# Optimization experiments

Measured on AMD Instinct MI355X. Metric: run time of the kernel, lower is better.

## Reference

```python
import jax, jax.numpy as jnp
import numpy as np

# Sinabs LIF semantics (norm_input=True default):
#   v[t] = alpha * v[t-1] + (1 - alpha) * x[t],  alpha = exp(-1/tau_mem)
#   spikes = MultiSpike: max(floor(v / threshold), 0)   (default sa.ActivationFunction)
#   reset  = MembraneSubtract: v -= spikes * threshold
# threshold_low=None -> no lower clamp.

TAU_MEM = 20.0
THRESHOLD = 1.0
GRAD_WIDTH = 0.5   # sinabs SingleExponential surrogate defaults
GRAD_SCALE = 1.0

@jax.custom_vjp
def spike_fn(v):
    # MultiSpike: number of threshold crossings this step
    return jnp.maximum(jnp.floor(v / THRESHOLD), 0.0)

def _spike_fwd(v):
    return spike_fn(v), v

def _spike_bwd(v, g):
    # single-exponential surrogate gradient around threshold
    sg = (GRAD_SCALE / GRAD_WIDTH) * jnp.exp(-jnp.abs(v - THRESHOLD) / GRAD_WIDTH)
    return (g * sg,)

spike_fn.defvjp(_spike_fwd, _spike_bwd)

def lif_layer(x):
    # x: [B, T, N] synaptic input; returns spikes [B, T, N]
    alpha = jnp.exp(jnp.asarray(-1.0 / TAU_MEM, dtype=x.dtype))
    one_m = 1.0 - alpha

    def step(v, xt):
        v = alpha * v + one_m * xt
        s = spike_fn(v)
        v = v - s * THRESHOLD  # membrane subtract reset
        return v, s

    v0 = jnp.zeros(x.shape[:1] + x.shape[2:], dtype=x.dtype)  # [B, N]
    _, spikes = jax.lax.scan(step, v0, jnp.swapaxes(x, 0, 1))  # scan over T
    return jnp.swapaxes(spikes, 0, 1)

def setup_inputs() -> dict:
    key = jax.random.key(0)
    k0, k1, k2, k3 = jax.random.split(key, 4)
    B, T, C_IN = 256, 4096, 16
    data = jax.random.normal(k0, (B, T, C_IN), dtype=jnp.float32)
    # nn.Linear(in, out, bias=False) weights are [out, in], kaiming-uniform-ish scale
    w1 = jax.random.normal(k1, (16, 16), dtype=jnp.float32) / np.sqrt(16)
    w2 = jax.random.normal(k2, (32, 16), dtype=jnp.float32) / np.sqrt(16)
    w3 = jax.random.normal(k3, (10, 32), dtype=jnp.float32) / np.sqrt(32)
    return {"data": data, "w1": w1, "w2": w2, "w3": w3}

def reference(data, w1, w2, w3):
    out = jnp.einsum('btc,oc->bto', data, w1)
    out = lif_layer(out)
    out = jnp.einsum('btc,oc->bto', out, w2)
    out = lif_layer(out)
    out = jnp.einsum('btc,oc->bto', out, w3)
    out = lif_layer(out)
    return out
```

## Files before the change

kernel.cpp:

```cpp
#include <hip/hip_runtime.h>
#include <stdint.h>
#include <math.h>

#define T_STEPS 4096
#define BATCH   256
#define NB_BLK  256

#define WAIT_VM0   0x0F70
#define WAIT_LGKM0 0xC07F

__device__ __forceinline__ float lif_step(float& v, float xs, float alpha) {
    float vp = fmaf(alpha, v, xs);
    float fr = vp - floorf(vp);
    float vn = fminf(vp, fr);
    float s  = vp - vn;
    v = vn;
    return s;
}

__device__ __forceinline__ float ubf(uint32_t w, int k) {
    return (float)((w >> (k * 8)) & 0xffu);
}

__device__ __forceinline__ float dot16(const float wr[16],
    float4 c0, float4 c1, float4 c2, float4 c3)
{
    float p0 = fmaf(wr[1], c0.y, wr[0] * c0.x);
    p0 = fmaf(wr[2], c0.z, p0);  p0 = fmaf(wr[3], c0.w, p0);
    float p1 = fmaf(wr[5], c1.y, wr[4] * c1.x);
    p1 = fmaf(wr[6], c1.z, p1);  p1 = fmaf(wr[7], c1.w, p1);
    float p2 = fmaf(wr[9], c2.y, wr[8] * c2.x);
    p2 = fmaf(wr[10], c2.z, p2); p2 = fmaf(wr[11], c2.w, p2);
    float p3 = fmaf(wr[13], c3.y, wr[12] * c3.x);
    p3 = fmaf(wr[14], c3.z, p3); p3 = fmaf(wr[15], c3.w, p3);
    return (p0 + p1) + (p2 + p3);
}

__device__ __forceinline__ void load_lds16(const float* g, float* l) {
    __builtin_amdgcn_global_load_lds(
        (const __attribute__((address_space(1))) void*)g,
        (__attribute__((address_space(3))) void*)l, 16, 0, 0);
}


__global__ __launch_bounds__(1024) void seg1(
    const float* __restrict__ x, const float* __restrict__ w1,
    float* __restrict__ out, uint8_t* __restrict__ s1t,
    uint8_t* __restrict__ bm1, uint8_t* __restrict__ bm2,
    uint8_t* __restrict__ flag1, uint8_t* __restrict__ flag2,
    float alpha, float one_m, float alpha16)
{
    const int tid = threadIdx.x;
    const int b   = blockIdx.x;

    __shared__ __align__(16) float xbuf[16640];
    __shared__ float   sh_end[NB_BLK][16];
    __shared__ float   sh_m0[NB_BLK][16];
    __shared__ float   sh_m1[NB_BLK][16];
    __shared__ uint8_t sh_badseg[16][NB_BLK];
    __shared__ int     sh_badch;
    __shared__ int     sh_spike;

    const int co = tid & 15;
    const int sg = tid >> 4;
    const int wv = tid >> 6;
    const int ln = tid & 63;

    const float* xb = x + (size_t)b * T_STEPS * 16;

#pragma unroll
    for (int q = 0; q < 4; ++q) {
        int s = wv * 4 + q;
        load_lds16(xb + (size_t)s * 256 + ln * 4, &xbuf[s * 260 + ln * 4]);
    }

    float4* o4 = (float4*)(out + (size_t)b * T_STEPS * 10);
    float4 z4 = make_float4(0.f, 0.f, 0.f, 0.f);
#pragma unroll
    for (int i = 0; i < 10; ++i) o4[i * 1024 + tid] = z4;
    if (tid < 16)
        ((uint4*)(bm1 + (size_t)b * NB_BLK))[tid] = make_uint4(0u,0u,0u,0u);
    else if (tid < 32)
        ((uint4*)(bm2 + (size_t)b * NB_BLK))[tid - 16] = make_uint4(0u,0u,0u,0u);
    else if (tid == 32) { flag2[b] = 0; sh_badch = 0; sh_spike = 0; }

    float wr[16];
#pragma unroll
    for (int i = 0; i < 16; ++i) wr[i] = one_m * w1[co * 16 + i];

    const int sbase = sg * 260;
    for (int k = 0; k < 4; ++k) {
        __builtin_amdgcn_s_waitcnt(WAIT_VM0);

        float acc = 0.0f, m0 = -1e30f, m1 = -1e30f, pw = alpha;
#pragma unroll
        for (int j = 0; j < 16; ++j) {
            const float* rp = &xbuf[sbase + j * 16];
            float4 c0 = *(const float4*)(rp + 0);
            float4 c1 = *(const float4*)(rp + 4);
            float4 c2 = *(const float4*)(rp + 8);
            float4 c3 = *(const float4*)(rp + 12);
            float y = dot16(wr, c0, c1, c2, c3);
            acc = fmaf(alpha, acc, y);
            m0  = fmaxf(m0, acc);
            m1  = fmaxf(m1, acc + pw);
            pw *= alpha;
        }
        const int gs = k * 64 + sg;
        sh_end[gs][co] = acc;
        sh_m0[gs][co]  = m0;
        sh_m1[gs][co]  = m1;

        if (k < 3) {
            __builtin_amdgcn_s_waitcnt(WAIT_LGKM0);
#pragma unroll
            for (int q = 0; q < 4; ++q) {
                int s = wv * 4 + q;
                load_lds16(xb + (size_t)((k + 1) * 64 + s) * 256 + ln * 4,
                           &xbuf[s * 260 + ln * 4]);
            }
        }
    }
    __syncthreads();

    if (tid < 16) {
        const int c = tid;
        float vs = 0.0f;
        int bad = 0;
#pragma unroll 8
        for (int s = 0; s < NB_BLK; ++s) {
            float vsu = fminf(fmaxf(vs + 1e-3f, 0.0f), 1.0f);
            float bound = fmaf(1.0f - vsu, sh_m0[s][c], vsu * sh_m1[s][c]);
            int sb = (bound >= 0.999f) ? 1 : 0;
            sh_badseg[c][s] = (uint8_t)sb;
            bad |= sb;
            vs = fmaf(alpha16, vs, sh_end[s][c]);
        }
        if (bad) atomicOr(&sh_badch, 1 << c);
    }
    __syncthreads();

    const int badmask = sh_badch;
    if (badmask) {
        uint4* sz = (uint4*)(s1t + (size_t)b * 16 * T_STEPS);
#pragma unroll
        for (int i = 0; i < 4; ++i) sz[i * 1024 + tid] = make_uint4(0u,0u,0u,0u);
        __syncthreads();

        int m = badmask;
        for (int i = 0; i < wv; ++i) m &= m - 1;
        if (ln == 0 && m) {
            const int c = __ffs(m) - 1;
            float wc[16];
#pragma unroll
            for (int i = 0; i < 16; ++i) wc[i] = one_m * w1[c * 16 + i];
            uint8_t* op  = s1t + ((size_t)b * 16 + c) * T_STEPS;
            uint8_t* bmp = bm1 + (size_t)b * NB_BLK;
            const uint8_t* bs = &sh_badseg[c][0];
            float v = 0.0f;
            int any = 0;
            for (int s = 0; s < NB_BLK; ++s) {
                if (!bs[s]) {
                    v = fmaf(alpha16, v, sh_end[s][c]);
                } else {
                    const float4* xq = (const float4*)xb + (size_t)s * 64;
                    uint32_t w[4] = {0u,0u,0u,0u};
#pragma unroll 4
                    for (int j = 0; j < 16; ++j) {
                        float4 c0 = xq[j*4+0], c1 = xq[j*4+1];
                        float4 c2 = xq[j*4+2], c3 = xq[j*4+3];
                        float y  = dot16(wc, c0, c1, c2, c3);
                        float sp = lif_step(v, y, alpha);
                        w[j >> 2] |= ((uint32_t)(int)sp) << ((j & 3) * 8);
                    }
                    if (w[0] | w[1] | w[2] | w[3]) {
                        *(uint4*)(op + s * 16) = make_uint4(w[0], w[1], w[2], w[3]);
                        bmp[s] = 1;
                        any = 1;
                    }
                }
            }
            if (any) sh_spike = 1;
        }
        __syncthreads();
    }
    if (tid == 0) flag1[b] = (uint8_t)sh_spike;
}

__global__ __launch_bounds__(64) void scan2(const uint8_t* __restrict__ s1t,
        const float* __restrict__ w2, uint8_t* __restrict__ s2t,
        const uint8_t* __restrict__ bm1, uint8_t* __restrict__ bm2,
        const uint8_t* __restrict__ flag1, uint8_t* __restrict__ flag2,
        float alpha, float one_m)
{
    const int tid = threadIdx.x;
    const int co  = tid & 31;
    const int b   = blockIdx.x * 2 + (tid >> 5);
    if (!flag1[b]) return;

    float wr[16];
#pragma unroll
    for (int i = 0; i < 16; ++i) wr[i] = one_m * w2[co * 16 + i];

    const uint8_t* sbase = s1t + (size_t)b * 16 * T_STEPS;
    uint4* op = (uint4*)(s2t + ((size_t)b * 32 + co) * T_STEPS);
    const uint4* bmv = (const uint4*)(bm1 + (size_t)b * NB_BLK);
    uint8_t* bm2p = bm2 + (size_t)b * NB_BLK;

    float v = 0.0f;
    for (int sb = 0; sb < 16; ++sb) {
        uint4 bm = bmv[sb];
        if ((bm.x | bm.y | bm.z | bm.w) == 0u) {
            if (v != 0.0f) {
                for (int blk = 0; blk < 16 && v != 0.0f; ++blk) {
#pragma unroll
                    for (int j = 0; j < 16; ++j) v *= alpha;
                }
            }
            continue;
        }
        for (int blk = 0; blk < 16; ++blk) {
            uint32_t d = (blk < 4) ? bm.x : (blk < 8) ? bm.y
                       : (blk < 12) ? bm.z : bm.w;
            uint32_t byte = (d >> ((blk & 3) * 8)) & 0xffu;
            if (byte == 0u) {
                if (v != 0.0f) {
#pragma unroll
                    for (int j = 0; j < 16; ++j) v *= alpha;
                }
                continue;
            }
            const int tb = sb * 16 + blk;
            const int t0 = tb * 16;
            uint4 S[16];
#pragma unroll
            for (int c = 0; c < 16; ++c)
                S[c] = *(const uint4*)(sbase + (size_t)c * T_STEPS + t0);
            uint32_t w[4] = {0u, 0u, 0u, 0u};
#pragma unroll
            for (int j = 0; j < 16; ++j) {
                float xv[16];
#pragma unroll
                for (int c = 0; c < 16; ++c) {
                    uint32_t dd = (j < 4) ? S[c].x : (j < 8) ? S[c].y
                                : (j < 12) ? S[c].z : S[c].w;
                    xv[c] = ubf(dd, j & 3);
                }
                float p0 = fmaf(wr[1], xv[1], wr[0] * xv[0]);
                p0 = fmaf(wr[2], xv[2], p0);   p0 = fmaf(wr[3], xv[3], p0);
                float p1 = fmaf(wr[5], xv[5], wr[4] * xv[4]);
                p1 = fmaf(wr[6], xv[6], p1);   p1 = fmaf(wr[7], xv[7], p1);
                float p2 = fmaf(wr[9], xv[9], wr[8] * xv[8]);
                p2 = fmaf(wr[10], xv[10], p2); p2 = fmaf(wr[11], xv[11], p2);
                float p3 = fmaf(wr[13], xv[13], wr[12] * xv[12]);
                p3 = fmaf(wr[14], xv[14], p3); p3 = fmaf(wr[15], xv[15], p3);
                float xs = (p0 + p1) + (p2 + p3);
                float s = lif_step(v, xs, alpha);
                w[j >> 2] |= ((uint32_t)(int)s) << ((j & 3) * 8);
            }
            op[tb] = make_uint4(w[0], w[1], w[2], w[3]);
            if (w[0] | w[1] | w[2] | w[3]) { bm2p[tb] = 1; flag2[b] = 1; }
        }
    }
}

__global__ __launch_bounds__(64) void scan3(const uint8_t* __restrict__ s2t,
        const float* __restrict__ w3, float* __restrict__ out,
        const uint8_t* __restrict__ bm2, const uint8_t* __restrict__ flag2,
        float alpha, float one_m)
{
    const int tid = threadIdx.x;
    const int co  = tid & 15;
    const int b   = blockIdx.x * 4 + (tid >> 4);
    if (!flag2[b]) return;
    const bool active = (co < 10);

    float wr[32];
#pragma unroll
    for (int i = 0; i < 32; ++i) wr[i] = active ? (one_m * w3[co * 32 + i]) : 0.0f;

    const uint8_t* sbase = s2t + (size_t)b * 32 * T_STEPS;
    const uint4* bmv = (const uint4*)(bm2 + (size_t)b * NB_BLK);
    float* ob = out + (size_t)b * T_STEPS * 10 + co;

    float v = 0.0f;
    for (int sb = 0; sb < 16; ++sb) {
        uint4 bm = bmv[sb];
        if ((bm.x | bm.y | bm.z | bm.w) == 0u) {
            if (v != 0.0f) {
                for (int blk = 0; blk < 16 && v != 0.0f; ++blk) {
#pragma unroll
                    for (int j = 0; j < 16; ++j) v *= alpha;
                }
            }
            continue;
        }
        for (int blk = 0; blk < 16; ++blk) {
            uint32_t d = (blk < 4) ? bm.x : (blk < 8) ? bm.y
                       : (blk < 12) ? bm.z : bm.w;
            uint32_t byte = (d >> ((blk & 3) * 8)) & 0xffu;
            if (byte == 0u) {
                if (v != 0.0f) {
#pragma unroll
                    for (int j = 0; j < 16; ++j) v *= alpha;
                }
                continue;
            }
            const int t0 = (sb * 16 + blk) * 16;
            uint4 S[32];
#pragma unroll
            for (int c = 0; c < 32; ++c)
                S[c] = *(const uint4*)(sbase + (size_t)c * T_STEPS + t0);
#pragma unroll
            for (int j = 0; j < 16; ++j) {
                float xv[32];
#pragma unroll
                for (int c = 0; c < 32; ++c) {
                    uint32_t dd = (j < 4) ? S[c].x : (j < 8) ? S[c].y
                                : (j < 12) ? S[c].z : S[c].w;
                    xv[c] = ubf(dd, j & 3);
                }
                float p0 = fmaf(wr[1], xv[1], wr[0] * xv[0]);
                p0 = fmaf(wr[2],  xv[2],  p0); p0 = fmaf(wr[3],  xv[3],  p0);
                p0 = fmaf(wr[4],  xv[4],  p0); p0 = fmaf(wr[5],  xv[5],  p0);
                p0 = fmaf(wr[6],  xv[6],  p0); p0 = fmaf(wr[7],  xv[7],  p0);
                float p1 = fmaf(wr[9], xv[9], wr[8] * xv[8]);
                p1 = fmaf(wr[10], xv[10], p1); p1 = fmaf(wr[11], xv[11], p1);
                p1 = fmaf(wr[12], xv[12], p1); p1 = fmaf(wr[13], xv[13], p1);
                p1 = fmaf(wr[14], xv[14], p1); p1 = fmaf(wr[15], xv[15], p1);
                float p2 = fmaf(wr[17], xv[17], wr[16] * xv[16]);
                p2 = fmaf(wr[18], xv[18], p2); p2 = fmaf(wr[19], xv[19], p2);
                p2 = fmaf(wr[20], xv[20], p2); p2 = fmaf(wr[21], xv[21], p2);
                p2 = fmaf(wr[22], xv[22], p2); p2 = fmaf(wr[23], xv[23], p2);
                float p3 = fmaf(wr[25], xv[25], wr[24] * xv[24]);
                p3 = fmaf(wr[26], xv[26], p3); p3 = fmaf(wr[27], xv[27], p3);
                p3 = fmaf(wr[28], xv[28], p3); p3 = fmaf(wr[29], xv[29], p3);
                p3 = fmaf(wr[30], xv[30], p3); p3 = fmaf(wr[31], xv[31], p3);
                float xs = (p0 + p1) + (p2 + p3);
                float s = lif_step(v, xs, alpha);
                if (active && s != 0.0f) ob[(size_t)(t0 + j) * 10] = s;
            }
        }
    }
}

extern "C" void kernel_launch(void* const* d_in, const int* in_sizes, int n_in,
                              void* d_out, int out_size, void* d_ws, size_t ws_size,
                              hipStream_t stream)
{
    const float* data = (const float*)d_in[0];
    const float* w1   = (const float*)d_in[1];
    const float* w2   = (const float*)d_in[2];
    const float* w3   = (const float*)d_in[3];
    float* out = (float*)d_out;

    uint8_t* ws    = (uint8_t*)d_ws;
    uint8_t* s1t   = ws;
    uint8_t* s2t   = ws + (16u << 20);
    uint8_t* bm1   = ws + (48u << 20);
    uint8_t* bm2   = bm1 + (64u << 10);
    uint8_t* flag1 = bm2 + (64u << 10);
    uint8_t* flag2 = flag1 + 256;

    const float alpha   = expf(-1.0f / 20.0f);
    const float one_m   = 1.0f - alpha;
    const float alpha16 = expf(-16.0f / 20.0f);

    seg1 <<<BATCH,   1024, 0, stream>>>(data, w1, out, s1t, bm1, bm2,
                                        flag1, flag2, alpha, one_m, alpha16);
    scan2<<<BATCH/2,   64, 0, stream>>>(s1t, w2, s2t, bm1, bm2, flag1, flag2,
                                        alpha, one_m);
    scan3<<<BATCH/4,   64, 0, stream>>>(s2t, w3, out, bm2, flag2, alpha, one_m);
}
```

Baseline: 174.2 us.

## Fuse three LIF layers into one kernel with 8-step segments and quantized bounds

Merges the three kernels into a single per-batch kernel. Layer-2 and layer-3 scans now run inside the same block after a barrier, and the block bitmaps and flags move from global memory into LDS. The layer-1 pass switches from 16-step to 8-step segments with a double-buffered, XOR-swizzled LDS prefetch, and stores the per-segment max bounds as 8-bit quantized values. The bad-segment classification is split across four thread groups that use a 20-segment warm-up instead of a full serial prefix. This removes two launches and the global bitmap traffic, but layers 2 and 3 now run on only 32 or 16 threads of a 1024-thread block, and the warm-up truncation and quantization of the bound check add correctness risk.

Measured after the change: 215.7 us. 1.24x slower.

```diff
diff --git a/kernel.cpp b/kernel.cpp
--- a/kernel.cpp
+++ b/kernel.cpp
@@ -5,9 +5,9 @@
 #define T_STEPS 4096
 #define BATCH   256
 #define NB_BLK  256
-
-#define WAIT_VM0   0x0F70
-#define WAIT_LGKM0 0xC07F
+#define SEG     8
+#define NSEG    512
+#define NCHUNK  8
 
 __device__ __forceinline__ float lif_step(float& v, float xs, float alpha) {
     float vp = fmaf(alpha, v, xs);
@@ -42,24 +42,24 @@
         (__attribute__((address_space(3))) void*)l, 16, 0, 0);
 }
 
-
-__global__ __launch_bounds__(1024) void seg1(
+__global__ __launch_bounds__(1024) void fused(
     const float* __restrict__ x, const float* __restrict__ w1,
+    const float* __restrict__ w2, const float* __restrict__ w3,
     float* __restrict__ out, uint8_t* __restrict__ s1t,
-    uint8_t* __restrict__ bm1, uint8_t* __restrict__ bm2,
-    uint8_t* __restrict__ flag1, uint8_t* __restrict__ flag2,
-    float alpha, float one_m, float alpha16)
+    uint8_t* __restrict__ s2t,
+    float alpha, float one_m, float alpha8)
 {
     const int tid = threadIdx.x;
     const int b   = blockIdx.x;
 
-    __shared__ __align__(16) float xbuf[16640];
-    __shared__ float   sh_end[NB_BLK][16];
-    __shared__ float   sh_m0[NB_BLK][16];
-    __shared__ float   sh_m1[NB_BLK][16];
-    __shared__ uint8_t sh_badseg[16][NB_BLK];
-    __shared__ int     sh_badch;
-    __shared__ int     sh_spike;
+    __shared__ __align__(16) float xbuf[2][8192];
+    __shared__ float    sh_end[NSEG][16];
+    __shared__ uint8_t  sh_q0[NSEG][16];
+    __shared__ uint8_t  sh_q1[NSEG][16];
+    __shared__ uint32_t sh_badseg[16][NSEG / 32];
+    __shared__ uint8_t  sh_bm1[NB_BLK];
+    __shared__ uint8_t  sh_bm2[NB_BLK];
+    __shared__ int      sh_badch, sh_spike, sh_flag2;
 
     const int co = tid & 15;
     const int sg = tid >> 4;
@@ -68,34 +68,43 @@
 
     const float* xb = x + (size_t)b * T_STEPS * 16;
 
-#pragma unroll
-    for (int q = 0; q < 4; ++q) {
-        int s = wv * 4 + q;
-        load_lds16(xb + (size_t)s * 256 + ln * 4, &xbuf[s * 260 + ln * 4]);
-    }
+    if (tid < 64)        ((uint32_t*)sh_bm1)[tid] = 0u;
+    else if (tid < 128)  ((uint32_t*)sh_bm2)[tid - 64] = 0u;
+    else if (tid == 128) { sh_badch = 0; sh_spike = 0; sh_flag2 = 0; }
 
     float4* o4 = (float4*)(out + (size_t)b * T_STEPS * 10);
     float4 z4 = make_float4(0.f, 0.f, 0.f, 0.f);
 #pragma unroll
     for (int i = 0; i < 10; ++i) o4[i * 1024 + tid] = z4;
-    if (tid < 16)
-        ((uint4*)(bm1 + (size_t)b * NB_BLK))[tid] = make_uint4(0u,0u,0u,0u);
-    else if (tid < 32)
-        ((uint4*)(bm2 + (size_t)b * NB_BLK))[tid - 16] = make_uint4(0u,0u,0u,0u);
-    else if (tid == 32) { flag2[b] = 0; sh_badch = 0; sh_spike = 0; }
 
     float wr[16];
 #pragma unroll
     for (int i = 0; i < 16; ++i) wr[i] = one_m * w1[co * 16 + i];
 
-    const int sbase = sg * 260;
-    for (int k = 0; k < 4; ++k) {
-        __builtin_amdgcn_s_waitcnt(WAIT_VM0);
-
+    const int s2a = (ln >> 5);
+    const int s2b = s2a + 2;
+    const int jj  = (ln >> 2) & 7;
+    const int qq  = ln & 3;
+    const int offA = wv * 512 + s2a * 128 + ((jj ^ s2a) << 4) + (qq << 2);
+    const int offB = wv * 512 + s2b * 128 + ((jj ^ s2b) << 4) + (qq << 2);
+    const int ldsA = wv * 512 + (ln << 2);
+    const int ldsB = wv * 512 + 256 + (ln << 2);
+
+    load_lds16(xb + offA, &xbuf[0][ldsA]);
+    load_lds16(xb + offB, &xbuf[0][ldsB]);
+    load_lds16(xb + 8192 + offA, &xbuf[1][ldsA]);
+    load_lds16(xb + 8192 + offB, &xbuf[1][ldsB]);
+
+    const int s23 = sg & 3;
+    for (int k = 0; k < NCHUNK; ++k) {
+        if (k < NCHUNK - 1) asm volatile("s_waitcnt vmcnt(2)" ::: "memory");
+        else                asm volatile("s_waitcnt vmcnt(0)" ::: "memory");
+
+        const float* seg = &xbuf[k & 1][sg << 7];
         float acc = 0.0f, m0 = -1e30f, m1 = -1e30f, pw = alpha;
 #pragma unroll
-        for (int j = 0; j < 16; ++j) {
-            const float* rp = &xbuf[sbase + j * 16];
+        for (int j = 0; j < SEG; ++j) {
+            const float* rp = seg + ((j ^ s23) << 4);
             float4 c0 = *(const float4*)(rp + 0);
             float4 c1 = *(const float4*)(rp + 4);
             float4 c2 = *(const float4*)(rp + 8);
@@ -108,33 +117,42 @@
         }
         const int gs = k * 64 + sg;
         sh_end[gs][co] = acc;
-        sh_m0[gs][co]  = m0;
-        sh_m1[gs][co]  = m1;
-
-        if (k < 3) {
-            __builtin_amdgcn_s_waitcnt(WAIT_LGKM0);
-#pragma unroll
-            for (int q = 0; q < 4; ++q) {
-                int s = wv * 4 + q;
-                load_lds16(xb + (size_t)((k + 1) * 64 + s) * 256 + ln * 4,
-                           &xbuf[s * 260 + ln * 4]);
-            }
+        int q0 = (int)ceilf(fmaf(m0, 102.0f, 102.0f));
+        int q1 = (int)ceilf(fmaf(m1, 102.0f, 102.0f));
+        q0 = q0 < 0 ? 0 : (q0 > 255 ? 255 : q0);
+        q1 = q1 < 0 ? 0 : (q1 > 255 ? 255 : q1);
+        sh_q0[gs][co] = (uint8_t)q0;
+        sh_q1[gs][co] = (uint8_t)q1;
+
+        if (k < NCHUNK - 2) {
+            asm volatile("s_waitcnt lgkmcnt(0)" ::: "memory");
+            const float* src = xb + (size_t)(k + 2) * 8192;
+            float* bp = xbuf[k & 1];
+            load_lds16(src + offA, bp + ldsA);
+            load_lds16(src + offB, bp + ldsB);
         }
     }
     __syncthreads();
 
-    if (tid < 16) {
-        const int c = tid;
+    if (tid < 64) {
+        const int c  = tid & 15;
+        const int qd = tid >> 4;
+        const int s_begin = qd * 128;
+        const int s_start = (qd == 0) ? 0 : s_begin - 20;
         float vs = 0.0f;
+        uint32_t badw = 0;
         int bad = 0;
-#pragma unroll 8
-        for (int s = 0; s < NB_BLK; ++s) {
-            float vsu = fminf(fmaxf(vs + 1e-3f, 0.0f), 1.0f);
-            float bound = fmaf(1.0f - vsu, sh_m0[s][c], vsu * sh_m1[s][c]);
-            int sb = (bound >= 0.999f) ? 1 : 0;
-            sh_badseg[c][s] = (uint8_t)sb;
-            bad |= sb;
-            vs = fmaf(alpha16, vs, sh_end[s][c]);
+        for (int s = s_start; s < s_begin + 128; ++s) {
+            if (s >= s_begin) {
+                int q0 = sh_q0[s][c], q1 = sh_q1[s][c];
+                float mm0 = (q0 == 255) ? 1e30f : fmaf((float)q0, 0.0098039216f, -1.0f);
+                float mm1 = (q1 == 255) ? 1e30f : fmaf((float)q1, 0.0098039216f, -1.0f);
+                float vsu = fminf(fmaxf(vs + 1e-3f, 0.0f), 1.0f);
+                float bound = fmaf(1.0f - vsu, mm0, vsu * mm1);
+                if (bound >= 0.999f) { badw |= 1u << (s & 31); bad = 1; }
+                if ((s & 31) == 31) { sh_badseg[c][s >> 5] = badw; badw = 0; }
+            }
+            vs = fmaf(alpha8, vs, sh_end[s][c]);
         }
         if (bad) atomicOr(&sh_badch, 1 << c);
     }
@@ -154,191 +172,170 @@
             float wc[16];
 #pragma unroll
             for (int i = 0; i < 16; ++i) wc[i] = one_m * w1[c * 16 + i];
-            uint8_t* op  = s1t + ((size_t)b * 16 + c) * T_STEPS;
-            uint8_t* bmp = bm1 + (size_t)b * NB_BLK;
-            const uint8_t* bs = &sh_badseg[c][0];
+            uint8_t* op = s1t + ((size_t)b * 16 + c) * T_STEPS;
             float v = 0.0f;
             int any = 0;
-            for (int s = 0; s < NB_BLK; ++s) {
-                if (!bs[s]) {
-                    v = fmaf(alpha16, v, sh_end[s][c]);
+            for (int s = 0; s < NSEG; ++s) {
+                if (!((sh_badseg[c][s >> 5] >> (s & 31)) & 1u)) {
+                    v = fmaf(alpha8, v, sh_end[s][c]);
                 } else {
-                    const float4* xq = (const float4*)xb + (size_t)s * 64;
-                    uint32_t w[4] = {0u,0u,0u,0u};
-#pragma unroll 4
-                    for (int j = 0; j < 16; ++j) {
-                        float4 c0 = xq[j*4+0], c1 = xq[j*4+1];
-                        float4 c2 = xq[j*4+2], c3 = xq[j*4+3];
-                        float y  = dot16(wc, c0, c1, c2, c3);
+                    const float* xr0 = xb + (size_t)s * 128;
+                    uint32_t sw0 = 0u, sw1 = 0u;
+#pragma unroll
+                    for (int j = 0; j < SEG; ++j) {
+                        const float4* xr = (const float4*)(xr0 + j * 16);
+                        float y  = dot16(wc, xr[0], xr[1], xr[2], xr[3]);
                         float sp = lif_step(v, y, alpha);
-                        w[j >> 2] |= ((uint32_t)(int)sp) << ((j & 3) * 8);
-                    }
-                    if (w[0] | w[1] | w[2] | w[3]) {
-                        *(uint4*)(op + s * 16) = make_uint4(w[0], w[1], w[2], w[3]);
-                        bmp[s] = 1;
+                        if (j < 4) sw0 |= ((uint32_t)(int)sp) << (j * 8);
+                        else       sw1 |= ((uint32_t)(int)sp) << ((j - 4) * 8);
+                    }
+                    if (sw0 | sw1) {
+                        *(uint2*)(op + s * 8) = make_uint2(sw0, sw1);
+                        sh_bm1[s >> 1] = 1;
                         any = 1;
                     }
                 }
             }
             if (any) sh_spike = 1;
         }
+    }
+    __syncthreads();
+
+    if (sh_spike) {
+        if (tid < 32) {
+            const int c2 = tid;
+            float wr2[16];
+#pragma unroll
+            for (int i = 0; i < 16; ++i) wr2[i] = one_m * w2[c2 * 16 + i];
+            const uint8_t* sb1 = s1t + (size_t)b * 16 * T_STEPS;
+            uint4* op2 = (uint4*)(s2t + ((size_t)b * 32 + c2) * T_STEPS);
+            const uint4* bmv = (const uint4*)sh_bm1;
+            float v = 0.0f;
+            for (int sb = 0; sb < 16; ++sb) {
+                uint4 bm = bmv[sb];
+                if ((bm.x | bm.y | bm.z | bm.w) == 0u) {
+                    if (v != 0.0f) {
+                        for (int blk = 0; blk < 16 && v != 0.0f; ++blk) {
+#pragma unroll
+                            for (int j = 0; j < 16; ++j) v *= alpha;
+                        }
+                    }
+                    continue;
+                }
+                for (int blk = 0; blk < 16; ++blk) {
+                    uint32_t d = (blk < 4) ? bm.x : (blk < 8) ? bm.y
+                               : (blk < 12) ? bm.z : bm.w;
+                    uint32_t byte = (d >> ((blk & 3) * 8)) & 0xffu;
+                    if (byte == 0u) {
+                        if (v != 0.0f) {
+#pragma unroll
+                            for (int j = 0; j < 16; ++j) v *= alpha;
+                        }
+                        continue;
+                    }
+                    const int tb = sb * 16 + blk;
+                    const int t0 = tb * 16;
+                    uint4 S[16];
+#pragma unroll
+                    for (int c = 0; c < 16; ++c)
+                        S[c] = *(const uint4*)(sb1 + (size_t)c * T_STEPS + t0);
+                    uint32_t w[4] = {0u, 0u, 0u, 0u};
+#pragma unroll
+                    for (int j = 0; j < 16; ++j) {
+                        float xv[16];
+#pragma unroll
+                        for (int c = 0; c < 16; ++c) {
+                            uint32_t dd = (j < 4) ? S[c].x : (j < 8) ? S[c].y
+                                        : (j < 12) ? S[c].z : S[c].w;
+                            xv[c] = ubf(dd, j & 3);
+                        }
+                        float p0 = fmaf(wr2[1], xv[1], wr2[0] * xv[0]);
+                        p0 = fmaf(wr2[2], xv[2], p0);   p0 = fmaf(wr2[3], xv[3], p0);
+                        float p1 = fmaf(wr2[5], xv[5], wr2[4] * xv[4]);
+                        p1 = fmaf(wr2[6], xv[6], p1);   p1 = fmaf(wr2[7], xv[7], p1);
+                        float p2 = fmaf(wr2[9], xv[9], wr2[8] * xv[8]);
+                        p2 = fmaf(wr2[10], xv[10], p2); p2 = fmaf(wr2[11], xv[11], p2);
+                        float p3 = fmaf(wr2[13], xv[13], wr2[12] * xv[12]);
+                        p3 = fmaf(wr2[14], xv[14], p3); p3 = fmaf(wr2[15], xv[15], p3);
+                        float xs = (p0 + p1) + (p2 + p3);
+                        float s = lif_step(v, xs, alpha);
+                        w[j >> 2] |= ((uint32_t)(int)s) << ((j & 3) * 8);
+                    }
+                    op2[tb] = make_uint4(w[0], w[1], w[2], w[3]);
+                    if (w[0] | w[1] | w[2] | w[3]) { sh_bm2[tb] = 1; sh_flag2 = 1; }
+                }
+            }
+        }
         __syncthreads();
-    }
-    if (tid == 0) flag1[b] = (uint8_t)sh_spike;
-}
-
-__global__ __launch_bounds__(64) void scan2(const uint8_t* __restrict__ s1t,
-        const float* __restrict__ w2, uint8_t* __restrict__ s2t,
-        const uint8_t* __restrict__ bm1, uint8_t* __restrict__ bm2,
-        const uint8_t* __restrict__ flag1, uint8_t* __restrict__ flag2,
-        float alpha, float one_m)
-{
-    const int tid = threadIdx.x;
-    const int co  = tid & 31;
-    const int b   = blockIdx.x * 2 + (tid >> 5);
-    if (!flag1[b]) return;
-
-    float wr[16];
-#pragma unroll
-    for (int i = 0; i < 16; ++i) wr[i] = one_m * w2[co * 16 + i];
-
-    const uint8_t* sbase = s1t + (size_t)b * 16 * T_STEPS;
-    uint4* op = (uint4*)(s2t + ((size_t)b * 32 + co) * T_STEPS);
-    const uint4* bmv = (const uint4*)(bm1 + (size_t)b * NB_BLK);
-    uint8_t* bm2p = bm2 + (size_t)b * NB_BLK;
-
-    float v = 0.0f;
-    for (int sb = 0; sb < 16; ++sb) {
-        uint4 bm = bmv[sb];
-        if ((bm.x | bm.y | bm.z | bm.w) == 0u) {
-            if (v != 0.0f) {
-                for (int blk = 0; blk < 16 && v != 0.0f; ++blk) {
-#pragma unroll
-                    for (int j = 0; j < 16; ++j) v *= alpha;
-                }
-            }
-            continue;
-        }
-        for (int blk = 0; blk < 16; ++blk) {
-            uint32_t d = (blk < 4) ? bm.x : (blk < 8) ? bm.y
-                       : (blk < 12) ? bm.z : bm.w;
-            uint32_t byte = (d >> ((blk & 3) * 8)) & 0xffu;
-            if (byte == 0u) {
-                if (v != 0.0f) {
-#pragma unroll
-                    for (int j = 0; j < 16; ++j) v *= alpha;
-                }
-                continue;
-            }
-            const int tb = sb * 16 + blk;
-            const int t0 = tb * 16;
-            uint4 S[16];
-#pragma unroll
-            for (int c = 0; c < 16; ++c)
-                S[c] = *(const uint4*)(sbase + (size_t)c * T_STEPS + t0);
-            uint32_t w[4] = {0u, 0u, 0u, 0u};
-#pragma unroll
-            for (int j = 0; j < 16; ++j) {
-                float xv[16];
-#pragma unroll
-                for (int c = 0; c < 16; ++c) {
-                    uint32_t dd = (j < 4) ? S[c].x : (j < 8) ? S[c].y
-                                : (j < 12) ? S[c].z : S[c].w;
-                    xv[c] = ubf(dd, j & 3);
-                }
-                float p0 = fmaf(wr[1], xv[1], wr[0] * xv[0]);
-                p0 = fmaf(wr[2], xv[2], p0);   p0 = fmaf(wr[3], xv[3], p0);
-                float p1 = fmaf(wr[5], xv[5], wr[4] * xv[4]);
-                p1 = fmaf(wr[6], xv[6], p1);   p1 = fmaf(wr[7], xv[7], p1);
-                float p2 = fmaf(wr[9], xv[9], wr[8] * xv[8]);
-                p2 = fmaf(wr[10], xv[10], p2); p2 = fmaf(wr[11], xv[11], p2);
-                float p3 = fmaf(wr[13], xv[13], wr[12] * xv[12]);
-                p3 = fmaf(wr[14], xv[14], p3); p3 = fmaf(wr[15], xv[15], p3);
-                float xs = (p0 + p1) + (p2 + p3);
-                float s = lif_step(v, xs, alpha);
-                w[j >> 2] |= ((uint32_t)(int)s) << ((j & 3) * 8);
-            }
-            op[tb] = make_uint4(w[0], w[1], w[2], w[3]);
-            if (w[0] | w[1] | w[2] | w[3]) { bm2p[tb] = 1; flag2[b] = 1; }
-        }
-    }
-}
-
-__global__ __launch_bounds__(64) void scan3(const uint8_t* __restrict__ s2t,
-        const float* __restrict__ w3, float* __restrict__ out,
-        const uint8_t* __restrict__ bm2, const uint8_t* __restrict__ flag2,
-        float alpha, float one_m)
-{
-    const int tid = threadIdx.x;
-    const int co  = tid & 15;
-    const int b   = blockIdx.x * 4 + (tid >> 4);
-    if (!flag2[b]) return;
-    const bool active = (co < 10);
-
-    float wr[32];
-#pragma unroll
-    for (int i = 0; i < 32; ++i) wr[i] = active ? (one_m * w3[co * 32 + i]) : 0.0f;
-
-    const uint8_t* sbase = s2t + (size_t)b * 32 * T_STEPS;
-    const uint4* bmv = (const uint4*)(bm2 + (size_t)b * NB_BLK);
-    float* ob = out + (size_t)b * T_STEPS * 10 + co;
-
-    float v = 0.0f;
-    for (int sb = 0; sb < 16; ++sb) {
-        uint4 bm = bmv[sb];
-        if ((bm.x | bm.y | bm.z | bm.w) == 0u) {
-            if (v != 0.0f) {
-                for (int blk = 0; blk < 16 && v != 0.0f; ++blk) {
-#pragma unroll
-                    for (int j = 0; j < 16; ++j) v *= alpha;
-                }
-            }
-            continue;
-        }
-        for (int blk = 0; blk < 16; ++blk) {
-            uint32_t d = (blk < 4) ? bm.x : (blk < 8) ? bm.y
-                       : (blk < 12) ? bm.z : bm.w;
-            uint32_t byte = (d >> ((blk & 3) * 8)) & 0xffu;
-            if (byte == 0u) {
-                if (v != 0.0f) {
-#pragma unroll
-                    for (int j = 0; j < 16; ++j) v *= alpha;
-                }
-                continue;
-            }
-            const int t0 = (sb * 16 + blk) * 16;
-            uint4 S[32];
-#pragma unroll
-            for (int c = 0; c < 32; ++c)
-                S[c] = *(const uint4*)(sbase + (size_t)c * T_STEPS + t0);
-#pragma unroll
-            for (int j = 0; j < 16; ++j) {
-                float xv[32];
-#pragma unroll
-                for (int c = 0; c < 32; ++c) {
-                    uint32_t dd = (j < 4) ? S[c].x : (j < 8) ? S[c].y
-                                : (j < 12) ? S[c].z : S[c].w;
-                    xv[c] = ubf(dd, j & 3);
-                }
-                float p0 = fmaf(wr[1], xv[1], wr[0] * xv[0]);
-                p0 = fmaf(wr[2],  xv[2],  p0); p0 = fmaf(wr[3],  xv[3],  p0);
-                p0 = fmaf(wr[4],  xv[4],  p0); p0 = fmaf(wr[5],  xv[5],  p0);
-                p0 = fmaf(wr[6],  xv[6],  p0); p0 = fmaf(wr[7],  xv[7],  p0);
-                float p1 = fmaf(wr[9], xv[9], wr[8] * xv[8]);
-                p1 = fmaf(wr[10], xv[10], p1); p1 = fmaf(wr[11], xv[11], p1);
-                p1 = fmaf(wr[12], xv[12], p1); p1 = fmaf(wr[13], xv[13], p1);
-                p1 = fmaf(wr[14], xv[14], p1); p1 = fmaf(wr[15], xv[15], p1);
-                float p2 = fmaf(wr[17], xv[17], wr[16] * xv[16]);
-                p2 = fmaf(wr[18], xv[18], p2); p2 = fmaf(wr[19], xv[19], p2);
-                p2 = fmaf(wr[20], xv[20], p2); p2 = fmaf(wr[21], xv[21], p2);
-                p2 = fmaf(wr[22], xv[22], p2); p2 = fmaf(wr[23], xv[23], p2);
-                float p3 = fmaf(wr[25], xv[25], wr[24] * xv[24]);
-                p3 = fmaf(wr[26], xv[26], p3); p3 = fmaf(wr[27], xv[27], p3);
-                p3 = fmaf(wr[28], xv[28], p3); p3 = fmaf(wr[29], xv[29], p3);
-                p3 = fmaf(wr[30], xv[30], p3); p3 = fmaf(wr[31], xv[31], p3);
-                float xs = (p0 + p1) + (p2 + p3);
-                float s = lif_step(v, xs, alpha);
-                if (active && s != 0.0f) ob[(size_t)(t0 + j) * 10] = s;
+
+        if (sh_flag2 && tid < 16) {
+            const int c3 = tid;
+            const bool active = (c3 < 10);
+            float wr3[32];
+#pragma unroll
+            for (int i = 0; i < 32; ++i)
+                wr3[i] = active ? (one_m * w3[c3 * 32 + i]) : 0.0f;
+            const uint8_t* sb2 = s2t + (size_t)b * 32 * T_STEPS;
+            const uint4* bmv2 = (const uint4*)sh_bm2;
+            float* ob = out + (size_t)b * T_STEPS * 10 + c3;
+            float v = 0.0f;
+            for (int sb = 0; sb < 16; ++sb) {
+                uint4 bm = bmv2[sb];
+                if ((bm.x | bm.y | bm.z | bm.w) == 0u) {
+                    if (v != 0.0f) {
+                        for (int blk = 0; blk < 16 && v != 0.0f; ++blk) {
+#pragma unroll
+                            for (int j = 0; j < 16; ++j) v *= alpha;
+                        }
+                    }
+                    continue;
+                }
+                for (int blk = 0; blk < 16; ++blk) {
+                    uint32_t d = (blk < 4) ? bm.x : (blk < 8) ? bm.y
+                               : (blk < 12) ? bm.z : bm.w;
+                    uint32_t byte = (d >> ((blk & 3) * 8)) & 0xffu;
+                    if (byte == 0u) {
+                        if (v != 0.0f) {
+#pragma unroll
+                            for (int j = 0; j < 16; ++j) v *= alpha;
+                        }
+                        continue;
+                    }
+                    const int t0 = (sb * 16 + blk) * 16;
+                    uint4 S[32];
+#pragma unroll
+                    for (int c = 0; c < 32; ++c)
+                        S[c] = *(const uint4*)(sb2 + (size_t)c * T_STEPS + t0);
+#pragma unroll
+                    for (int j = 0; j < 16; ++j) {
+                        float xv[32];
+#pragma unroll
+                        for (int c = 0; c < 32; ++c) {
+                            uint32_t dd = (j < 4) ? S[c].x : (j < 8) ? S[c].y
+                                        : (j < 12) ? S[c].z : S[c].w;
+                            xv[c] = ubf(dd, j & 3);
+                        }
+                        float p0 = fmaf(wr3[1], xv[1], wr3[0] * xv[0]);
+                        p0 = fmaf(wr3[2],  xv[2],  p0); p0 = fmaf(wr3[3],  xv[3],  p0);
+                        p0 = fmaf(wr3[4],  xv[4],  p0); p0 = fmaf(wr3[5],  xv[5],  p0);
+                        p0 = fmaf(wr3[6],  xv[6],  p0); p0 = fmaf(wr3[7],  xv[7],  p0);
+                        float p1 = fmaf(wr3[9], xv[9], wr3[8] * xv[8]);
+                        p1 = fmaf(wr3[10], xv[10], p1); p1 = fmaf(wr3[11], xv[11], p1);
+                        p1 = fmaf(wr3[12], xv[12], p1); p1 = fmaf(wr3[13], xv[13], p1);
+                        p1 = fmaf(wr3[14], xv[14], p1); p1 = fmaf(wr3[15], xv[15], p1);
+                        float p2 = fmaf(wr3[17], xv[17], wr3[16] * xv[16]);
+                        p2 = fmaf(wr3[18], xv[18], p2); p2 = fmaf(wr3[19], xv[19], p2);
+                        p2 = fmaf(wr3[20], xv[20], p2); p2 = fmaf(wr3[21], xv[21], p2);
+                        p2 = fmaf(wr3[22], xv[22], p2); p2 = fmaf(wr3[23], xv[23], p2);
+                        float p3 = fmaf(wr3[25], xv[25], wr3[24] * xv[24]);
+                        p3 = fmaf(wr3[26], xv[26], p3); p3 = fmaf(wr3[27], xv[27], p3);
+                        p3 = fmaf(wr3[28], xv[28], p3); p3 = fmaf(wr3[29], xv[29], p3);
+                        p3 = fmaf(wr3[30], xv[30], p3); p3 = fmaf(wr3[31], xv[31], p3);
+                        float xs = (p0 + p1) + (p2 + p3);
+                        float s = lif_step(v, xs, alpha);
+                        if (active && s != 0.0f) ob[(size_t)(t0 + j) * 10] = s;
+                    }
+                }
             }
         }
     }
@@ -354,21 +351,14 @@
     const float* w3   = (const float*)d_in[3];
     float* out = (float*)d_out;
 
-    uint8_t* ws    = (uint8_t*)d_ws;
-    uint8_t* s1t   = ws;
-    uint8_t* s2t   = ws + (16u << 20);
-    uint8_t* bm1   = ws + (48u << 20);
-    uint8_t* bm2   = bm1 + (64u << 10);
-    uint8_t* flag1 = bm2 + (64u << 10);
-    uint8_t* flag2 = flag1 + 256;
-
-    const float alpha   = expf(-1.0f / 20.0f);
-    const float one_m   = 1.0f - alpha;
-    const float alpha16 = expf(-16.0f / 20.0f);
-
-    seg1 <<<BATCH,   1024, 0, stream>>>(data, w1, out, s1t, bm1, bm2,
-                                        flag1, flag2, alpha, one_m, alpha16);
-    scan2<<<BATCH/2,   64, 0, stream>>>(s1t, w2, s2t, bm1, bm2, flag1, flag2,
-                                        alpha, one_m);
-    scan3<<<BATCH/4,   64, 0, stream>>>(s2t, w3, out, bm2, flag2, alpha, one_m);
-}
+    uint8_t* ws  = (uint8_t*)d_ws;
+    uint8_t* s1t = ws;
+    uint8_t* s2t = ws + (16u << 20);
+
+    const float alpha  = expf(-1.0f / 20.0f);
+    const float one_m  = 1.0f - alpha;
+    const float alpha8 = expf(-8.0f / 20.0f);
+
+    fused<<<BATCH, 1024, 0, stream>>>(data, w1, w2, w3, out, s1t, s2t,
+                                      alpha, one_m, alpha8);
+}
```
